# Kernel tuning notes

Measured on AMD Instinct MI355X. Metric: run time of the kernel, lower is better.

The kernel has to match this reference:

```python
import jax, jax.numpy as jnp
import numpy as np

N_NODES = 100000
N_GRAPHS = 64


def _gcn_norm(edge_index, num_nodes):
    # Add self-loops and compute symmetric normalization (PyG GCNConv gcn_norm).
    src = jnp.concatenate([edge_index[0], jnp.arange(num_nodes, dtype=edge_index.dtype)])
    dst = jnp.concatenate([edge_index[1], jnp.arange(num_nodes, dtype=edge_index.dtype)])
    deg = jax.ops.segment_sum(jnp.ones_like(dst, dtype=jnp.float32), dst, num_segments=num_nodes)
    dinv = jnp.where(deg > 0, jax.lax.rsqrt(deg), 0.0)
    norm = dinv[src] * dinv[dst]  # [E + N]
    return src, dst, norm


def _gcn_conv(x, src, dst, norm, W, b, num_nodes):
    h = x @ W                                   # [N, out]
    msg = h[src] * norm[:, None]                # gather + scale  [E+N, out]
    out = jax.ops.segment_sum(msg, dst, num_segments=num_nodes)  # scatter-add
    return out + b


def setup_inputs() -> dict:
    key = jax.random.key(0)
    ks = jax.random.split(key, 8)
    E = 1600000
    pos = jax.random.normal(ks[0], (N_NODES, 3), dtype=jnp.float32)
    edge_index = jax.random.randint(ks[1], (2, E), 0, N_NODES, dtype=jnp.int64)
    batch = jnp.sort(jax.random.randint(ks[2], (N_NODES,), 0, N_GRAPHS, dtype=jnp.int64))
    def glorot(k, shape):
        lim = np.sqrt(6.0 / (shape[0] + shape[1])).astype(np.float32)
        return jax.random.uniform(k, shape, dtype=jnp.float32, minval=-lim, maxval=lim)
    return {
        "pos": pos,
        "edge_index": edge_index,
        "batch": batch,
        "W1": glorot(ks[3], (3, 64)),  "b1": jnp.zeros((64,), jnp.float32),
        "W2": glorot(ks[4], (64, 64)), "b2": jnp.zeros((64,), jnp.float32),
        "W3": glorot(ks[5], (64, 24)), "b3": jnp.zeros((24,), jnp.float32),
    }


def reference(pos, edge_index, batch, W1, b1, W2, b2, W3, b3):
    src, dst, norm = _gcn_norm(edge_index, N_NODES)
    h = jax.nn.relu(_gcn_conv(pos, src, dst, norm, W1, b1, N_NODES))
    h = jax.nn.relu(_gcn_conv(h, src, dst, norm, W2, b2, N_NODES))
    y = _gcn_conv(h, src, dst, norm, W3, b3, N_NODES)  # [N, 24]
    # global_mean_pool over batch ids, then tanh
    sums = jax.ops.segment_sum(y, batch, num_segments=N_GRAPHS)          # [G, 24]
    counts = jax.ops.segment_sum(jnp.ones((N_NODES,), jnp.float32), batch, num_segments=N_GRAPHS)
    mean = sums / jnp.maximum(counts, 1.0)[:, None]
    return jnp.tanh(mean)
```

## Files before the change

### kernel.cpp

```cpp
#include <hip/hip_runtime.h>
#include <math.h>

#define NNODES 100000
#define NGRAPHS 64
#define NB 391
#define CAP 4608
#define NBLKA 1024
#define NBLKB 512


__device__ __forceinline__ unsigned int f2bf(float x) {
    union { float f; unsigned int u; } v;
    v.f = x;
    unsigned int r = v.u + 0x7FFFu + ((v.u >> 16) & 1u);
    return r >> 16;
}
__device__ __forceinline__ unsigned int pack2bf(float lo, float hi) {
    return f2bf(lo) | (f2bf(hi) << 16);
}
__device__ __forceinline__ float bflo(unsigned int u) {
    union { unsigned int u; float f; } v;
    v.u = u << 16;
    return v.f;
}
__device__ __forceinline__ float bfhi(unsigned int u) {
    union { unsigned int u; float f; } v;
    v.u = u & 0xFFFF0000u;
    return v.f;
}


__device__ __forceinline__ int ntld(const int* p) { return __builtin_nontemporal_load(p); }
__device__ __forceinline__ int2 ntld2(const int2* p) {
    long long v = __builtin_nontemporal_load((const long long*)p);
    int2 r;
    r.x = (int)(unsigned int)(v & 0xffffffffLL);
    r.y = (int)(v >> 32);
    return r;
}


__global__ void bucket_scatter(const int* __restrict__ src, const int* __restrict__ dst,
                               int* __restrict__ bCur, unsigned int* __restrict__ packed,
                               int E) {
    __shared__ int h[NB];
    __shared__ int cur[NB];
    for (int k = threadIdx.x; k < NB; k += 256) h[k] = 0;
    __syncthreads();
    int base = blockIdx.x * 2048 + threadIdx.x;
    int d[8], s[8], b[8];
#pragma unroll
    for (int k = 0; k < 8; ++k) {
        int e = base + k * 256;
        if (e < E) {
            d[k] = dst[e];
            s[k] = src[e];
            b[k] = d[k] >> 8;
            atomicAdd(&h[b[k]], 1);
        }
    }
    __syncthreads();
    for (int k = threadIdx.x; k < NB; k += 256) {
        int c = h[k];
        cur[k] = c ? atomicAdd(&bCur[k], c) : 0;
    }
    __syncthreads();
#pragma unroll
    for (int k = 0; k < 8; ++k) {
        int e = base + k * 256;
        if (e < E) {
            int pos = atomicAdd(&cur[b[k]], 1);
            if (pos < CAP)
                packed[(size_t)b[k] * CAP + pos] = ((unsigned int)(d[k] & 255) << 17) | (unsigned int)s[k];
        }
    }
}

__global__ void bucket_build(const unsigned int* __restrict__ packed, const int* __restrict__ bCur,
                             const int* __restrict__ batch, const float* __restrict__ pos,
                             int2* __restrict__ rowBE, int* __restrict__ col,
                             float* __restrict__ dinv, int2* __restrict__ dg,
                             float4* __restrict__ pos4, int N_) {
    __shared__ int cnt[256];
    __shared__ int bas[256];
    int tid = threadIdx.x;
    int b = blockIdx.x;
    int count = bCur[b];
    if (count > CAP) count = CAP;
    int beg = b * CAP;
    cnt[tid] = 0;
    __syncthreads();
    for (int k = beg + tid; k < beg + count; k += 256) atomicAdd(&cnt[packed[k] >> 17], 1);
    __syncthreads();
    int myCnt = cnt[tid];
    bas[tid] = myCnt;
    __syncthreads();
    for (int off = 1; off < 256; off <<= 1) {
        int v = (tid >= off) ? bas[tid - off] : 0;
        __syncthreads();
        bas[tid] += v;
        __syncthreads();
    }
    int excl = beg + ((tid > 0) ? bas[tid - 1] : 0);
    int node = (b << 8) + tid;
    if (node < N_) {
        rowBE[node] = make_int2(excl, excl + myCnt);
        float di = rsqrtf((float)myCnt + 1.0f);
        dinv[node] = di;
        dg[node] = make_int2(__float_as_int(di), batch[node]);
        pos4[node] = make_float4(pos[node * 3] * di, pos[node * 3 + 1] * di,
                                 pos[node * 3 + 2] * di, di);
    }
    __syncthreads();
    bas[tid] = excl;
    __syncthreads();
    for (int k = beg + tid; k < beg + count; k += 256) {
        unsigned int p = packed[k];
        int pos_ = atomicAdd(&bas[p >> 17], 1);
        col[pos_] = (int)(p & 0x1FFFFu);
    }
}


__global__ void mm12_gp(const float4* __restrict__ pos4, const int2* __restrict__ rowBE,
                        const int* __restrict__ col, const float* __restrict__ dinv,
                        const float* __restrict__ W1, const float* __restrict__ b1,
                        const float* __restrict__ W2, uint2* __restrict__ outb, int n) {
    __shared__ float4 part[256];
    __shared__ float4 ag[64];
    __shared__ float xs[64][65];
    __shared__ float4 ws[64 * 16];
    const int tid = threadIdx.x;
    const int rowBase = blockIdx.x * 64;
    const int r = tid >> 2, t4 = tid & 3;
    const int i = rowBase + r;

    float sx = 0, sy = 0, sz = 0, dival = 0;
    if (i < n) {
        int2 be = rowBE[i];
        float4 ps = pos4[i];
        dival = ps.w;
        if (t4 == 0) { sx = ps.x; sy = ps.y; sz = ps.z; }
        for (int j = be.x + t4; j < be.y; j += 4) {
            float4 v = pos4[ntld(&col[j])];
            sx += v.x; sy += v.y; sz += v.z;
        }
    }
    part[tid] = make_float4(sx, sy, sz, dival);
    const float4* W24 = (const float4*)W2;
    for (int idx = tid; idx < 64 * 16; idx += 256) ws[idx] = W24[idx];
    __syncthreads();
    if (tid < 64) {
        float4 p0 = part[tid * 4], p1 = part[tid * 4 + 1];
        float4 p2 = part[tid * 4 + 2], p3 = part[tid * 4 + 3];
        ag[tid] = make_float4((p0.x + p1.x) + (p2.x + p3.x),
                              (p0.y + p1.y) + (p2.y + p3.y),
                              (p0.z + p1.z) + (p2.z + p3.z), p0.w);
    }
    __syncthreads();
    for (int idx = tid; idx < 64 * 64; idx += 256) {
        int rr = idx >> 6;
        int k = idx & 63;
        float4 a = ag[rr];
        float v = b1[k] + a.w * (a.x * W1[k] + a.y * W1[64 + k] + a.z * W1[128 + k]);
        xs[rr][k] = fmaxf(v, 0.0f);
    }
    __syncthreads();

    const int f4 = tid & 15;
    const int r0 = (tid >> 4) * 4;
    float4 a0 = make_float4(0, 0, 0, 0), a1 = a0, a2 = a0, a3 = a0;
#pragma unroll 4
    for (int k = 0; k < 64; ++k) {
        float4 wv = ws[k * 16 + f4];
        float xa = xs[r0 + 0][k];
        float xb = xs[r0 + 1][k];
        float xc = xs[r0 + 2][k];
        float xd = xs[r0 + 3][k];
        a0.x += wv.x * xa; a0.y += wv.y * xa; a0.z += wv.z * xa; a0.w += wv.w * xa;
        a1.x += wv.x * xb; a1.y += wv.y * xb; a1.z += wv.z * xb; a1.w += wv.w * xb;
        a2.x += wv.x * xc; a2.y += wv.y * xc; a2.z += wv.z * xc; a2.w += wv.w * xc;
        a3.x += wv.x * xd; a3.y += wv.y * xd; a3.z += wv.z * xd; a3.w += wv.w * xd;
    }
    int i0 = rowBase + r0;
    float d0 = (i0 + 0 < n) ? dinv[i0 + 0] : 1.0f;
    float d1 = (i0 + 1 < n) ? dinv[i0 + 1] : 1.0f;
    float d2 = (i0 + 2 < n) ? dinv[i0 + 2] : 1.0f;
    float d3 = (i0 + 3 < n) ? dinv[i0 + 3] : 1.0f;
    if (i0 + 0 < n)
        outb[(size_t)(i0 + 0) * 16 + f4] = make_uint2(pack2bf(a0.x * d0, a0.y * d0), pack2bf(a0.z * d0, a0.w * d0));
    if (i0 + 1 < n)
        outb[(size_t)(i0 + 1) * 16 + f4] = make_uint2(pack2bf(a1.x * d1, a1.y * d1), pack2bf(a1.z * d1, a1.w * d1));
    if (i0 + 2 < n)
        outb[(size_t)(i0 + 2) * 16 + f4] = make_uint2(pack2bf(a2.x * d2, a2.y * d2), pack2bf(a2.z * d2, a2.w * d2));
    if (i0 + 3 < n)
        outb[(size_t)(i0 + 3) * 16 + f4] = make_uint2(pack2bf(a3.x * d3, a3.y * d3), pack2bf(a3.z * d3, a3.w * d3));
}


__global__ void gather2_b16(const int2* __restrict__ rowBE, const int* __restrict__ col,
                            const uint4* __restrict__ h, const float* __restrict__ dinv,
                            const float* __restrict__ bias, uint4* __restrict__ outb, int n) {
    int t = blockIdx.x * blockDim.x + threadIdx.x;
    if (t >= n * 8) return;
    int i = t >> 3;
    int c8 = t & 7;
    float di = dinv[i];
    int2 be = rowBE[i];
    float acc[8];
    {
        uint4 sv = h[t];
        acc[0] = bflo(sv.x); acc[1] = bfhi(sv.x);
        acc[2] = bflo(sv.y); acc[3] = bfhi(sv.y);
        acc[4] = bflo(sv.z); acc[5] = bfhi(sv.z);
        acc[6] = bflo(sv.w); acc[7] = bfhi(sv.w);
    }
    int j = be.x;
    for (; j + 8 <= be.y; j += 8) {
        int s[8];
        uint4 v[8];
#pragma unroll
        for (int k = 0; k < 8; ++k) s[k] = ntld(&col[j + k]);
#pragma unroll
        for (int k = 0; k < 8; ++k) v[k] = h[(size_t)s[k] * 8 + c8];
#pragma unroll
        for (int k = 0; k < 8; ++k) {
            acc[0] += bflo(v[k].x); acc[1] += bfhi(v[k].x);
            acc[2] += bflo(v[k].y); acc[3] += bfhi(v[k].y);
            acc[4] += bflo(v[k].z); acc[5] += bfhi(v[k].z);
            acc[6] += bflo(v[k].w); acc[7] += bfhi(v[k].w);
        }
    }
    for (; j < be.y; ++j) {
        uint4 v = h[(size_t)ntld(&col[j]) * 8 + c8];
        acc[0] += bflo(v.x); acc[1] += bfhi(v.x);
        acc[2] += bflo(v.y); acc[3] += bfhi(v.y);
        acc[4] += bflo(v.z); acc[5] += bfhi(v.z);
        acc[6] += bflo(v.w); acc[7] += bfhi(v.w);
    }
    const float* bv = bias + c8 * 8;
#pragma unroll
    for (int k = 0; k < 8; ++k) acc[k] = fmaxf(acc[k] * di + bv[k], 0.0f);
    outb[t] = make_uint4(pack2bf(acc[0], acc[1]), pack2bf(acc[2], acc[3]),
                         pack2bf(acc[4], acc[5]), pack2bf(acc[6], acc[7]));
}


__device__ __forceinline__ void st_y(uint2* __restrict__ yA, uint2* __restrict__ yB,
                                     int i, int f4, uint2 v) {
    if (f4 < 4) yA[(size_t)i * 4 + f4] = v;
    else        yB[(size_t)i * 2 + (f4 - 4)] = v;
}

__global__ void mm3_b16(const uint4* __restrict__ xb, const float* __restrict__ W,
                        const float* __restrict__ dinv, uint2* __restrict__ yA,
                        uint2* __restrict__ yB, int n) {
    __shared__ float xs[128][65];
    __shared__ float4 ws[64 * 6];
    const int tid = threadIdx.x;
    const int rowBase = blockIdx.x * 128;

    for (int idx = tid; idx < 128 * 8; idx += 192) {
        int r = idx >> 3;
        int c8 = idx & 7;
        int gr = rowBase + r;
        uint4 v = (gr < n) ? xb[(size_t)gr * 8 + c8] : make_uint4(0, 0, 0, 0);
        float* xp = &xs[r][c8 * 8];
        xp[0] = bflo(v.x); xp[1] = bfhi(v.x);
        xp[2] = bflo(v.y); xp[3] = bfhi(v.y);
        xp[4] = bflo(v.z); xp[5] = bfhi(v.z);
        xp[6] = bflo(v.w); xp[7] = bfhi(v.w);
    }
    const float4* W4 = (const float4*)W;
    for (int idx = tid; idx < 64 * 6; idx += 192) ws[idx] = W4[idx];
    __syncthreads();

    const int f4 = tid % 6;
    const int r0 = (tid / 6) * 4;
    float4 a0 = make_float4(0, 0, 0, 0), a1 = a0, a2 = a0, a3 = a0;
#pragma unroll 4
    for (int k = 0; k < 64; ++k) {
        float4 wv = ws[k * 6 + f4];
        float xa = xs[r0 + 0][k];
        float xb_ = xs[r0 + 1][k];
        float xc = xs[r0 + 2][k];
        float xd = xs[r0 + 3][k];
        a0.x += wv.x * xa; a0.y += wv.y * xa; a0.z += wv.z * xa; a0.w += wv.w * xa;
        a1.x += wv.x * xb_; a1.y += wv.y * xb_; a1.z += wv.z * xb_; a1.w += wv.w * xb_;
        a2.x += wv.x * xc; a2.y += wv.y * xc; a2.z += wv.z * xc; a2.w += wv.w * xc;
        a3.x += wv.x * xd; a3.y += wv.y * xd; a3.z += wv.z * xd; a3.w += wv.w * xd;
    }
    int i0 = rowBase + r0;
    float d0 = (i0 + 0 < n) ? dinv[i0 + 0] : 1.0f;
    float d1 = (i0 + 1 < n) ? dinv[i0 + 1] : 1.0f;
    float d2 = (i0 + 2 < n) ? dinv[i0 + 2] : 1.0f;
    float d3 = (i0 + 3 < n) ? dinv[i0 + 3] : 1.0f;
    if (i0 + 0 < n)
        st_y(yA, yB, i0 + 0, f4, make_uint2(pack2bf(a0.x * d0, a0.y * d0), pack2bf(a0.z * d0, a0.w * d0)));
    if (i0 + 1 < n)
        st_y(yA, yB, i0 + 1, f4, make_uint2(pack2bf(a1.x * d1, a1.y * d1), pack2bf(a1.z * d1, a1.w * d1)));
    if (i0 + 2 < n)
        st_y(yA, yB, i0 + 2, f4, make_uint2(pack2bf(a2.x * d2, a2.y * d2), pack2bf(a2.z * d2, a2.w * d2)));
    if (i0 + 3 < n)
        st_y(yA, yB, i0 + 3, f4, make_uint2(pack2bf(a3.x * d3, a3.y * d3), pack2bf(a3.z * d3, a3.w * d3)));
}


__global__ void gather3A(const int2* __restrict__ rowBE, const int* __restrict__ col,
                         const uint4* __restrict__ yA, const int2* __restrict__ dg,
                         float* __restrict__ partA) {
    __shared__ float lpool[NGRAPHS * 16];
    for (int k = threadIdx.x; k < NGRAPHS * 16; k += 256) lpool[k] = 0.0f;
    __syncthreads();

    const int T = NNODES * 4;
    const int stride = NBLKA * 256;
    for (int t = blockIdx.x * 256 + threadIdx.x; t < T; t += stride) {
        int i = t >> 2;
        int half = t & 1;
        int r = (t >> 1) & 1;
        int2 wi = ntld2(&dg[i]);
        float di = __int_as_float(wi.x);
        int g = wi.y;
        int2 be = ntld2(&rowBE[i]);
        int mid = be.x + ((be.y - be.x + 1) >> 1);
        int a = half ? mid : be.x;
        int b = half ? be.y : mid;
        float acc[8] = {0, 0, 0, 0, 0, 0, 0, 0};
        if (!half) {
            uint4 sv = yA[(size_t)i * 2 + r];
            acc[0] = bflo(sv.x); acc[1] = bfhi(sv.x);
            acc[2] = bflo(sv.y); acc[3] = bfhi(sv.y);
            acc[4] = bflo(sv.z); acc[5] = bfhi(sv.z);
            acc[6] = bflo(sv.w); acc[7] = bfhi(sv.w);
        }
        int j = a;
        for (; j + 8 <= b; j += 8) {
            int s[8];
            uint4 v[8];
#pragma unroll
            for (int k = 0; k < 8; ++k) s[k] = ntld(&col[j + k]);
#pragma unroll
            for (int k = 0; k < 8; ++k) v[k] = yA[(size_t)s[k] * 2 + r];
#pragma unroll
            for (int k = 0; k < 8; ++k) {
                acc[0] += bflo(v[k].x); acc[1] += bfhi(v[k].x);
                acc[2] += bflo(v[k].y); acc[3] += bfhi(v[k].y);
                acc[4] += bflo(v[k].z); acc[5] += bfhi(v[k].z);
                acc[6] += bflo(v[k].w); acc[7] += bfhi(v[k].w);
            }
        }
        for (; j < b; ++j) {
            uint4 v = yA[(size_t)ntld(&col[j]) * 2 + r];
            acc[0] += bflo(v.x); acc[1] += bfhi(v.x);
            acc[2] += bflo(v.y); acc[3] += bfhi(v.y);
            acc[4] += bflo(v.z); acc[5] += bfhi(v.z);
            acc[6] += bflo(v.w); acc[7] += bfhi(v.w);
        }
#pragma unroll
        for (int k = 0; k < 8; ++k) acc[k] += __shfl_xor(acc[k], 1);
        if (!half) {
            float* lp = &lpool[g * 16 + r * 8];
#pragma unroll
            for (int k = 0; k < 8; ++k) atomicAdd(&lp[k], acc[k] * di);
        }
    }
    __syncthreads();
    float* pp = partA + (size_t)blockIdx.x * (NGRAPHS * 16);
    for (int k = threadIdx.x; k < NGRAPHS * 16; k += 256) pp[k] = lpool[k];
}

__global__ void gather3B(const int2* __restrict__ rowBE, const int* __restrict__ col,
                         const uint4* __restrict__ yB, const int2* __restrict__ dg,
                         float* __restrict__ partB, float* __restrict__ cpart) {
    __shared__ float lpool[NGRAPHS * 8];
    __shared__ float lcnt[NGRAPHS];
    for (int k = threadIdx.x; k < NGRAPHS * 8; k += 256) lpool[k] = 0.0f;
    for (int k = threadIdx.x; k < NGRAPHS; k += 256) lcnt[k] = 0.0f;
    __syncthreads();

    const int T = NNODES * 2;
    const int stride = NBLKB * 256;
    for (int t = blockIdx.x * 256 + threadIdx.x; t < T; t += stride) {
        int i = t >> 1;
        int half = t & 1;
        int2 wi = ntld2(&dg[i]);
        float di = __int_as_float(wi.x);
        int g = wi.y;
        int2 be = ntld2(&rowBE[i]);
        int mid = be.x + ((be.y - be.x + 1) >> 1);
        int a = half ? mid : be.x;
        int b = half ? be.y : mid;
        float acc[8] = {0, 0, 0, 0, 0, 0, 0, 0};
        if (!half) {
            uint4 sv = yB[i];
            acc[0] = bflo(sv.x); acc[1] = bfhi(sv.x);
            acc[2] = bflo(sv.y); acc[3] = bfhi(sv.y);
            acc[4] = bflo(sv.z); acc[5] = bfhi(sv.z);
            acc[6] = bflo(sv.w); acc[7] = bfhi(sv.w);
        }
        int j = a;
        for (; j + 8 <= b; j += 8) {
            int s[8];
            uint4 v[8];
#pragma unroll
            for (int k = 0; k < 8; ++k) s[k] = ntld(&col[j + k]);
#pragma unroll
            for (int k = 0; k < 8; ++k) v[k] = yB[s[k]];
#pragma unroll
            for (int k = 0; k < 8; ++k) {
                acc[0] += bflo(v[k].x); acc[1] += bfhi(v[k].x);
                acc[2] += bflo(v[k].y); acc[3] += bfhi(v[k].y);
                acc[4] += bflo(v[k].z); acc[5] += bfhi(v[k].z);
                acc[6] += bflo(v[k].w); acc[7] += bfhi(v[k].w);
            }
        }
        for (; j < b; ++j) {
            uint4 v = yB[ntld(&col[j])];
            acc[0] += bflo(v.x); acc[1] += bfhi(v.x);
            acc[2] += bflo(v.y); acc[3] += bfhi(v.y);
            acc[4] += bflo(v.z); acc[5] += bfhi(v.z);
            acc[6] += bflo(v.w); acc[7] += bfhi(v.w);
        }
#pragma unroll
        for (int k = 0; k < 8; ++k) acc[k] += __shfl_xor(acc[k], 1);
        if (!half) {
            float* lp = &lpool[g * 8];
#pragma unroll
            for (int k = 0; k < 8; ++k) atomicAdd(&lp[k], acc[k] * di);
            atomicAdd(&lcnt[g], 1.0f);
        }
    }
    __syncthreads();
    float* pp = partB + (size_t)blockIdx.x * (NGRAPHS * 8);
    for (int k = threadIdx.x; k < NGRAPHS * 8; k += 256) pp[k] = lpool[k];
    float* cp = cpart + (size_t)blockIdx.x * NGRAPHS;
    for (int k = threadIdx.x; k < NGRAPHS; k += 256) cp[k] = lcnt[k];
}

__global__ void pool_finish(const float* __restrict__ partA, const float* __restrict__ partB,
                            const float* __restrict__ cpart, const float* __restrict__ b3,
                            float* __restrict__ out) {
    int w = blockIdx.x * 4 + (threadIdx.x >> 6);
    int lane = threadIdx.x & 63;
    if (w >= NGRAPHS * 24) return;
    int g = w / 24;
    int c = w - g * 24;
    float s = 0.0f, cn = 0.0f;
    if (c < 16) {
        for (int b = lane; b < NBLKA; b += 64) s += partA[(size_t)b * (NGRAPHS * 16) + g * 16 + c];
    } else {
        for (int b = lane; b < NBLKB; b += 64) s += partB[(size_t)b * (NGRAPHS * 8) + g * 8 + (c - 16)];
    }
    for (int b = lane; b < NBLKB; b += 64) cn += cpart[(size_t)b * NGRAPHS + g];
#pragma unroll
    for (int off = 32; off > 0; off >>= 1) {
        s += __shfl_down(s, off);
        cn += __shfl_down(cn, off);
    }
    if (lane == 0) out[w] = tanhf(s / fmaxf(cn, 1.0f) + b3[c]);
}


static inline int gridFor(long long total, int block) {
    return (int)((total + block - 1) / block);
}

extern "C" void kernel_launch(void* const* d_in, const int* in_sizes, int n_in,
                              void* d_out, int out_size, void* d_ws, size_t ws_size,
                              hipStream_t stream) {
    const float* pos   = (const float*)d_in[0];
    const int*   ei    = (const int*)d_in[1];
    const int*   batch = (const int*)d_in[2];
    const float* W1    = (const float*)d_in[3];
    const float* b1    = (const float*)d_in[4];
    const float* W2    = (const float*)d_in[5];
    const float* b2    = (const float*)d_in[6];
    const float* W3    = (const float*)d_in[7];
    const float* b3    = (const float*)d_in[8];
    float*       out   = (float*)d_out;

    const int N = NNODES;
    const int E = in_sizes[1] / 2;
    const int* src = ei;
    const int* dst = ei + E;

    char* p = (char*)d_ws;
    uint4*  z2b    = (uint4*)p;         p += (size_t)N * 8 * sizeof(uint4);
    uint4*  h2b    = (uint4*)p;         p += (size_t)N * 8 * sizeof(uint4);
    uint4*  yA     = (uint4*)p;         p += (size_t)N * 2 * sizeof(uint4);
    uint4*  yB     = (uint4*)p;         p += (size_t)N * 1 * sizeof(uint4);
    float4* pos4   = (float4*)p;        p += (size_t)N * sizeof(float4);
    int2*   rowBE  = (int2*)p;          p += (size_t)N * sizeof(int2);
    int2*   dg     = (int2*)p;          p += (size_t)N * sizeof(int2);
    float*  dinv   = (float*)p;         p += (size_t)N * sizeof(float);
    int*    bCur   = (int*)p;           p += NB * sizeof(int);
    unsigned int* packed = (unsigned int*)p;  p += (size_t)NB * CAP * sizeof(unsigned int);
    int*    col    = (int*)p;           p += (size_t)NB * CAP * sizeof(int);
    float*  partA  = (float*)z2b;
    float*  partB  = partA + (size_t)NBLKA * NGRAPHS * 16;
    float*  cpartB = partB + (size_t)NBLKB * NGRAPHS * 8;

    const int B = 256;
    const int edgeBlocks = gridFor(E, 2048);

    hipMemsetAsync(bCur, 0, NB * sizeof(int), stream);
    bucket_scatter<<<edgeBlocks, 256, 0, stream>>>(src, dst, bCur, packed, E);
    bucket_build<<<NB, 256, 0, stream>>>(packed, bCur, batch, pos, rowBE, col, dinv, dg, pos4, N);

    mm12_gp<<<gridFor(N, 64), 256, 0, stream>>>(pos4, rowBE, col, dinv, W1, b1, W2, (uint2*)z2b, N);

    gather2_b16<<<gridFor((long long)N * 8, B), B, 0, stream>>>(rowBE, col, z2b, dinv, b2, h2b, N);

    mm3_b16<<<gridFor(N, 128), 192, 0, stream>>>(h2b, W3, dinv, (uint2*)yA, (uint2*)yB, N);
    gather3A<<<NBLKA, 256, 0, stream>>>(rowBE, col, yA, dg, partA);
    gather3B<<<NBLKB, 256, 0, stream>>>(rowBE, col, yB, dg, partB, cpartB);
    pool_finish<<<gridFor((long long)NGRAPHS * 24 * 64, B), B, 0, stream>>>(partA, partB, cpartB, b3, out);
}
```

Measured before the change: 265.3 us.

## Fuse layer-2 gather with layer-3 matmul via shared-memory tile

Merges the layer-2 neighbor aggregation and the layer-3 64x24 projection into one kernel. Each 256-thread block aggregates 32 nodes, writes the ReLU outputs to shared memory, then 192 threads compute the W3 projection and store the bf16 yA/yB outputs. This drops the h2b intermediate's global write and reread and one kernel launch. In exchange it adds a block barrier after the irregular gather and a small per-block W3 load, and it removes the bounds check, which relies on N*8 being a multiple of 256.

After: 256.9 us, median of 3. 1.03x faster.

```diff
diff --git a/kernel.cpp b/kernel.cpp
--- a/kernel.cpp
+++ b/kernel.cpp
@@ -198,15 +198,28 @@
 }
 
 
-__global__ void gather2_b16(const int2* __restrict__ rowBE, const int* __restrict__ col,
+__device__ __forceinline__ void st_y(uint2* __restrict__ yA, uint2* __restrict__ yB,
+                                     int i, int f4, uint2 v) {
+    if (f4 < 4) yA[(size_t)i * 4 + f4] = v;
+    else        yB[(size_t)i * 2 + (f4 - 4)] = v;
+}
+
+__global__ void gather2_mm3(const int2* __restrict__ rowBE, const int* __restrict__ col,
                             const uint4* __restrict__ h, const float* __restrict__ dinv,
-                            const float* __restrict__ bias, uint4* __restrict__ outb, int n) {
-    int t = blockIdx.x * blockDim.x + threadIdx.x;
-    if (t >= n * 8) return;
-    int i = t >> 3;
-    int c8 = t & 7;
-    float di = dinv[i];
-    int2 be = rowBE[i];
+                            const float* __restrict__ bias, const float* __restrict__ W3,
+                            uint2* __restrict__ yA, uint2* __restrict__ yB) {
+    __shared__ float hs[32][65];
+    __shared__ float dd[32];
+    __shared__ float w3s[64 * 24];
+    const int tid = threadIdx.x;
+    for (int idx = tid; idx < 64 * 24 / 4; idx += 256)
+        ((float4*)w3s)[idx] = ((const float4*)W3)[idx];
+
+    const int t = blockIdx.x * 256 + tid;
+    const int i = t >> 3;
+    const int c8 = t & 7;
+    const float di = dinv[i];
+    const int2 be = rowBE[i];
     float acc[8];
     {
         uint4 sv = h[t];
@@ -238,71 +251,35 @@
         acc[4] += bflo(v.z); acc[5] += bfhi(v.z);
         acc[6] += bflo(v.w); acc[7] += bfhi(v.w);
     }
-    const float* bv = bias + c8 * 8;
-#pragma unroll
-    for (int k = 0; k < 8; ++k) acc[k] = fmaxf(acc[k] * di + bv[k], 0.0f);
-    outb[t] = make_uint4(pack2bf(acc[0], acc[1]), pack2bf(acc[2], acc[3]),
-                         pack2bf(acc[4], acc[5]), pack2bf(acc[6], acc[7]));
-}
-
-
-__device__ __forceinline__ void st_y(uint2* __restrict__ yA, uint2* __restrict__ yB,
-                                     int i, int f4, uint2 v) {
-    if (f4 < 4) yA[(size_t)i * 4 + f4] = v;
-    else        yB[(size_t)i * 2 + (f4 - 4)] = v;
-}
-
-__global__ void mm3_b16(const uint4* __restrict__ xb, const float* __restrict__ W,
-                        const float* __restrict__ dinv, uint2* __restrict__ yA,
-                        uint2* __restrict__ yB, int n) {
-    __shared__ float xs[128][65];
-    __shared__ float4 ws[64 * 6];
-    const int tid = threadIdx.x;
-    const int rowBase = blockIdx.x * 128;
-
-    for (int idx = tid; idx < 128 * 8; idx += 192) {
-        int r = idx >> 3;
-        int c8 = idx & 7;
-        int gr = rowBase + r;
-        uint4 v = (gr < n) ? xb[(size_t)gr * 8 + c8] : make_uint4(0, 0, 0, 0);
-        float* xp = &xs[r][c8 * 8];
-        xp[0] = bflo(v.x); xp[1] = bfhi(v.x);
-        xp[2] = bflo(v.y); xp[3] = bfhi(v.y);
-        xp[4] = bflo(v.z); xp[5] = bfhi(v.z);
-        xp[6] = bflo(v.w); xp[7] = bfhi(v.w);
-    }
-    const float4* W4 = (const float4*)W;
-    for (int idx = tid; idx < 64 * 6; idx += 192) ws[idx] = W4[idx];
-    __syncthreads();
-
-    const int f4 = tid % 6;
-    const int r0 = (tid / 6) * 4;
-    float4 a0 = make_float4(0, 0, 0, 0), a1 = a0, a2 = a0, a3 = a0;
+    const int il = tid >> 3;
+    {
+        const float* bv = bias + c8 * 8;
+        float* hp = &hs[il][c8 * 8];
+#pragma unroll
+        for (int k = 0; k < 8; ++k) hp[k] = fmaxf(acc[k] * di + bv[k], 0.0f);
+        if (c8 == 0) dd[il] = di;
+    }
+    __syncthreads();
+
+    if (tid < 192) {
+        const int node = tid / 6;
+        const int f4 = tid - node * 6;
+        const int gi = blockIdx.x * 32 + node;
+        const float dloc = dd[node];
+        const float* hrow = hs[node];
+        const float* wp = &w3s[f4 * 4];
+        float c0 = 0, c1 = 0, c2 = 0, c3 = 0;
 #pragma unroll 4
-    for (int k = 0; k < 64; ++k) {
-        float4 wv = ws[k * 6 + f4];
-        float xa = xs[r0 + 0][k];
-        float xb_ = xs[r0 + 1][k];
-        float xc = xs[r0 + 2][k];
-        float xd = xs[r0 + 3][k];
-        a0.x += wv.x * xa; a0.y += wv.y * xa; a0.z += wv.z * xa; a0.w += wv.w * xa;
-        a1.x += wv.x * xb_; a1.y += wv.y * xb_; a1.z += wv.z * xb_; a1.w += wv.w * xb_;
-        a2.x += wv.x * xc; a2.y += wv.y * xc; a2.z += wv.z * xc; a2.w += wv.w * xc;
-        a3.x += wv.x * xd; a3.y += wv.y * xd; a3.z += wv.z * xd; a3.w += wv.w * xd;
-    }
-    int i0 = rowBase + r0;
-    float d0 = (i0 + 0 < n) ? dinv[i0 + 0] : 1.0f;
-    float d1 = (i0 + 1 < n) ? dinv[i0 + 1] : 1.0f;
-    float d2 = (i0 + 2 < n) ? dinv[i0 + 2] : 1.0f;
-    float d3 = (i0 + 3 < n) ? dinv[i0 + 3] : 1.0f;
-    if (i0 + 0 < n)
-        st_y(yA, yB, i0 + 0, f4, make_uint2(pack2bf(a0.x * d0, a0.y * d0), pack2bf(a0.z * d0, a0.w * d0)));
-    if (i0 + 1 < n)
-        st_y(yA, yB, i0 + 1, f4, make_uint2(pack2bf(a1.x * d1, a1.y * d1), pack2bf(a1.z * d1, a1.w * d1)));
-    if (i0 + 2 < n)
-        st_y(yA, yB, i0 + 2, f4, make_uint2(pack2bf(a2.x * d2, a2.y * d2), pack2bf(a2.z * d2, a2.w * d2)));
-    if (i0 + 3 < n)
-        st_y(yA, yB, i0 + 3, f4, make_uint2(pack2bf(a3.x * d3, a3.y * d3), pack2bf(a3.z * d3, a3.w * d3)));
+        for (int k = 0; k < 64; ++k) {
+            float hv = hrow[k];
+            c0 += hv * wp[k * 24 + 0];
+            c1 += hv * wp[k * 24 + 1];
+            c2 += hv * wp[k * 24 + 2];
+            c3 += hv * wp[k * 24 + 3];
+        }
+        st_y(yA, yB, gi, f4, make_uint2(pack2bf(c0 * dloc, c1 * dloc),
+                                        pack2bf(c2 * dloc, c3 * dloc)));
+    }
 }
 
 
@@ -487,7 +464,6 @@
 
     char* p = (char*)d_ws;
     uint4*  z2b    = (uint4*)p;         p += (size_t)N * 8 * sizeof(uint4);
-    uint4*  h2b    = (uint4*)p;         p += (size_t)N * 8 * sizeof(uint4);
     uint4*  yA     = (uint4*)p;         p += (size_t)N * 2 * sizeof(uint4);
     uint4*  yB     = (uint4*)p;         p += (size_t)N * 1 * sizeof(uint4);
     float4* pos4   = (float4*)p;        p += (size_t)N * sizeof(float4);
@@ -510,9 +486,9 @@
 
     mm12_gp<<<gridFor(N, 64), 256, 0, stream>>>(pos4, rowBE, col, dinv, W1, b1, W2, (uint2*)z2b, N);
 
-    gather2_b16<<<gridFor((long long)N * 8, B), B, 0, stream>>>(rowBE, col, z2b, dinv, b2, h2b, N);
-
-    mm3_b16<<<gridFor(N, 128), 192, 0, stream>>>(h2b, W3, dinv, (uint2*)yA, (uint2*)yB, N);
+    gather2_mm3<<<gridFor((long long)N * 8, B), B, 0, stream>>>(rowBE, col, z2b, dinv, b2, W3,
+                                                                (uint2*)yA, (uint2*)yB);
+
     gather3A<<<NBLKA, 256, 0, stream>>>(rowBE, col, yA, dg, partA);
     gather3B<<<NBLKB, 256, 0, stream>>>(rowBE, col, yB, dg, partB, cpartB);
     pool_finish<<<gridFor((long long)NGRAPHS * 24 * 64, B), B, 0, stream>>>(partA, partB, cpartB, b3, out);
```

## Slice layer-2 features into four 16-channel planes for cache-local gathers

Applied to the files above, without the earlier changes.

The layer-2 intermediate is stored as four separate 16-channel bf16 planes, each node-major, instead of one interleaved 64-channel row. The new gather kernel processes one plane per grid slice, with four threads per node splitting the edge list and reducing through shuffles. Each plane is 3.2 MB, so the random neighbour gathers can hit in cache instead of streaming the full 12.8 MB array. The cost is reading the edge list four times and an extra shuffle reduction. The producer mm12 and consumer mm3 kernels are updated to the sliced layout.

Result: slower. 287.6 us (+8.4%).

```diff
diff --git a/kernel.cpp b/kernel.cpp
--- a/kernel.cpp
+++ b/kernel.cpp
@@ -7,6 +7,7 @@
 #define CAP 4608
 #define NBLKA 1024
 #define NBLKB 512
+#define NT2 1563
 
 
 __device__ __forceinline__ unsigned int f2bf(float x) {
@@ -28,6 +29,12 @@
     v.u = u & 0xFFFF0000u;
     return v.f;
 }
+
+#define ACC8(A, ofs, V) \
+    A[(ofs) + 0] += bflo((V).x); A[(ofs) + 1] += bfhi((V).x); \
+    A[(ofs) + 2] += bflo((V).y); A[(ofs) + 3] += bfhi((V).y); \
+    A[(ofs) + 4] += bflo((V).z); A[(ofs) + 5] += bfhi((V).z); \
+    A[(ofs) + 6] += bflo((V).w); A[(ofs) + 7] += bfhi((V).w);
 
 
 __device__ __forceinline__ int ntld(const int* p) { return __builtin_nontemporal_load(p); }
@@ -125,7 +132,7 @@
 __global__ void mm12_gp(const float4* __restrict__ pos4, const int2* __restrict__ rowBE,
                         const int* __restrict__ col, const float* __restrict__ dinv,
                         const float* __restrict__ W1, const float* __restrict__ b1,
-                        const float* __restrict__ W2, uint2* __restrict__ outb, int n) {
+                        const float* __restrict__ W2, uint2* __restrict__ outz, int n) {
     __shared__ float4 part[256];
     __shared__ float4 ag[64];
     __shared__ float xs[64][65];
@@ -187,62 +194,78 @@
     float d1 = (i0 + 1 < n) ? dinv[i0 + 1] : 1.0f;
     float d2 = (i0 + 2 < n) ? dinv[i0 + 2] : 1.0f;
     float d3 = (i0 + 3 < n) ? dinv[i0 + 3] : 1.0f;
+    const size_t gsel = (size_t)(f4 >> 2) * NNODES;
+    const int sub = f4 & 3;
     if (i0 + 0 < n)
-        outb[(size_t)(i0 + 0) * 16 + f4] = make_uint2(pack2bf(a0.x * d0, a0.y * d0), pack2bf(a0.z * d0, a0.w * d0));
+        outz[(gsel + (i0 + 0)) * 4 + sub] = make_uint2(pack2bf(a0.x * d0, a0.y * d0), pack2bf(a0.z * d0, a0.w * d0));
     if (i0 + 1 < n)
-        outb[(size_t)(i0 + 1) * 16 + f4] = make_uint2(pack2bf(a1.x * d1, a1.y * d1), pack2bf(a1.z * d1, a1.w * d1));
+        outz[(gsel + (i0 + 1)) * 4 + sub] = make_uint2(pack2bf(a1.x * d1, a1.y * d1), pack2bf(a1.z * d1, a1.w * d1));
     if (i0 + 2 < n)
-        outb[(size_t)(i0 + 2) * 16 + f4] = make_uint2(pack2bf(a2.x * d2, a2.y * d2), pack2bf(a2.z * d2, a2.w * d2));
+        outz[(gsel + (i0 + 2)) * 4 + sub] = make_uint2(pack2bf(a2.x * d2, a2.y * d2), pack2bf(a2.z * d2, a2.w * d2));
     if (i0 + 3 < n)
-        outb[(size_t)(i0 + 3) * 16 + f4] = make_uint2(pack2bf(a3.x * d3, a3.y * d3), pack2bf(a3.z * d3, a3.w * d3));
-}
-
-
-__global__ void gather2_b16(const int2* __restrict__ rowBE, const int* __restrict__ col,
-                            const uint4* __restrict__ h, const float* __restrict__ dinv,
-                            const float* __restrict__ bias, uint4* __restrict__ outb, int n) {
-    int t = blockIdx.x * blockDim.x + threadIdx.x;
-    if (t >= n * 8) return;
-    int i = t >> 3;
-    int c8 = t & 7;
-    float di = dinv[i];
-    int2 be = rowBE[i];
-    float acc[8];
-    {
-        uint4 sv = h[t];
-        acc[0] = bflo(sv.x); acc[1] = bfhi(sv.x);
-        acc[2] = bflo(sv.y); acc[3] = bfhi(sv.y);
-        acc[4] = bflo(sv.z); acc[5] = bfhi(sv.z);
-        acc[6] = bflo(sv.w); acc[7] = bfhi(sv.w);
-    }
-    int j = be.x;
-    for (; j + 8 <= be.y; j += 8) {
-        int s[8];
-        uint4 v[8];
-#pragma unroll
-        for (int k = 0; k < 8; ++k) s[k] = ntld(&col[j + k]);
-#pragma unroll
-        for (int k = 0; k < 8; ++k) v[k] = h[(size_t)s[k] * 8 + c8];
-#pragma unroll
-        for (int k = 0; k < 8; ++k) {
-            acc[0] += bflo(v[k].x); acc[1] += bfhi(v[k].x);
-            acc[2] += bflo(v[k].y); acc[3] += bfhi(v[k].y);
-            acc[4] += bflo(v[k].z); acc[5] += bfhi(v[k].z);
-            acc[6] += bflo(v[k].w); acc[7] += bfhi(v[k].w);
-        }
-    }
-    for (; j < be.y; ++j) {
-        uint4 v = h[(size_t)ntld(&col[j]) * 8 + c8];
-        acc[0] += bflo(v.x); acc[1] += bfhi(v.x);
-        acc[2] += bflo(v.y); acc[3] += bfhi(v.y);
-        acc[4] += bflo(v.z); acc[5] += bfhi(v.z);
-        acc[6] += bflo(v.w); acc[7] += bfhi(v.w);
-    }
-    const float* bv = bias + c8 * 8;
-#pragma unroll
-    for (int k = 0; k < 8; ++k) acc[k] = fmaxf(acc[k] * di + bv[k], 0.0f);
-    outb[t] = make_uint4(pack2bf(acc[0], acc[1]), pack2bf(acc[2], acc[3]),
-                         pack2bf(acc[4], acc[5]), pack2bf(acc[6], acc[7]));
+        outz[(gsel + (i0 + 3)) * 4 + sub] = make_uint2(pack2bf(a3.x * d3, a3.y * d3), pack2bf(a3.z * d3, a3.w * d3));
+}
+
+
+__global__ void gather2_sliced(const int2* __restrict__ rowBE, const int* __restrict__ col,
+                               const uint4* __restrict__ z2s, const float* __restrict__ dinv,
+                               const float* __restrict__ b2, uint4* __restrict__ h2s) {
+    const int tid = threadIdx.x;
+    const int g = blockIdx.x / NT2;
+    const int tile = blockIdx.x - g * NT2;
+    const int il = tid >> 2, t4 = tid & 3;
+    const int i = tile * 64 + il;
+    const size_t base = (size_t)g * NNODES;
+
+    float acc[16];
+#pragma unroll
+    for (int k = 0; k < 16; ++k) acc[k] = 0.0f;
+
+    if (i < NNODES) {
+        if (t4 == 0) {
+            uint4 sa = z2s[(base + i) * 2 + 0];
+            uint4 sb = z2s[(base + i) * 2 + 1];
+            ACC8(acc, 0, sa)
+            ACC8(acc, 8, sb)
+        }
+        int2 be = rowBE[i];
+        int j = be.x + t4;
+        for (; j + 4 < be.y; j += 8) {
+            int s0 = ntld(&col[j]);
+            int s1 = ntld(&col[j + 4]);
+            uint4 a0 = z2s[(base + s0) * 2 + 0];
+            uint4 b0 = z2s[(base + s0) * 2 + 1];
+            uint4 a1 = z2s[(base + s1) * 2 + 0];
+            uint4 b1 = z2s[(base + s1) * 2 + 1];
+            ACC8(acc, 0, a0)
+            ACC8(acc, 8, b0)
+            ACC8(acc, 0, a1)
+            ACC8(acc, 8, b1)
+        }
+        for (; j < be.y; j += 4) {
+            int s = ntld(&col[j]);
+            uint4 a = z2s[(base + s) * 2 + 0];
+            uint4 b = z2s[(base + s) * 2 + 1];
+            ACC8(acc, 0, a)
+            ACC8(acc, 8, b)
+        }
+    }
+#pragma unroll
+    for (int k = 0; k < 16; ++k) acc[k] += __shfl_xor(acc[k], 1);
+#pragma unroll
+    for (int k = 0; k < 16; ++k) acc[k] += __shfl_xor(acc[k], 2);
+
+    if (t4 == 0 && i < NNODES) {
+        float di = dinv[i];
+        const float* bv = b2 + g * 16;
+        float h[16];
+#pragma unroll
+        for (int k = 0; k < 16; ++k) h[k] = fmaxf(acc[k] * di + bv[k], 0.0f);
+        h2s[(base + i) * 2 + 0] = make_uint4(pack2bf(h[0], h[1]), pack2bf(h[2], h[3]),
+                                             pack2bf(h[4], h[5]), pack2bf(h[6], h[7]));
+        h2s[(base + i) * 2 + 1] = make_uint4(pack2bf(h[8], h[9]), pack2bf(h[10], h[11]),
+                                             pack2bf(h[12], h[13]), pack2bf(h[14], h[15]));
+    }
 }
 
 
@@ -264,7 +287,8 @@
         int r = idx >> 3;
         int c8 = idx & 7;
         int gr = rowBase + r;
-        uint4 v = (gr < n) ? xb[(size_t)gr * 8 + c8] : make_uint4(0, 0, 0, 0);
+        uint4 v = (gr < n) ? xb[((size_t)(c8 >> 1) * NNODES + gr) * 2 + (c8 & 1)]
+                           : make_uint4(0, 0, 0, 0);
         float* xp = &xs[r][c8 * 8];
         xp[0] = bflo(v.x); xp[1] = bfhi(v.x);
         xp[2] = bflo(v.y); xp[3] = bfhi(v.y);
@@ -486,8 +510,8 @@
     const int* dst = ei + E;
 
     char* p = (char*)d_ws;
-    uint4*  z2b    = (uint4*)p;         p += (size_t)N * 8 * sizeof(uint4);
-    uint4*  h2b    = (uint4*)p;         p += (size_t)N * 8 * sizeof(uint4);
+    uint4*  z2s    = (uint4*)p;         p += (size_t)N * 8 * sizeof(uint4);
+    uint4*  h2s    = (uint4*)p;         p += (size_t)N * 8 * sizeof(uint4);
     uint4*  yA     = (uint4*)p;         p += (size_t)N * 2 * sizeof(uint4);
     uint4*  yB     = (uint4*)p;         p += (size_t)N * 1 * sizeof(uint4);
     float4* pos4   = (float4*)p;        p += (size_t)N * sizeof(float4);
@@ -497,7 +521,7 @@
     int*    bCur   = (int*)p;           p += NB * sizeof(int);
     unsigned int* packed = (unsigned int*)p;  p += (size_t)NB * CAP * sizeof(unsigned int);
     int*    col    = (int*)p;           p += (size_t)NB * CAP * sizeof(int);
-    float*  partA  = (float*)z2b;
+    float*  partA  = (float*)z2s;
     float*  partB  = partA + (size_t)NBLKA * NGRAPHS * 16;
     float*  cpartB = partB + (size_t)NBLKB * NGRAPHS * 8;
 
@@ -508,11 +532,12 @@
     bucket_scatter<<<edgeBlocks, 256, 0, stream>>>(src, dst, bCur, packed, E);
     bucket_build<<<NB, 256, 0, stream>>>(packed, bCur, batch, pos, rowBE, col, dinv, dg, pos4, N);
 
-    mm12_gp<<<gridFor(N, 64), 256, 0, stream>>>(pos4, rowBE, col, dinv, W1, b1, W2, (uint2*)z2b, N);
-
-    gather2_b16<<<gridFor((long long)N * 8, B), B, 0, stream>>>(rowBE, col, z2b, dinv, b2, h2b, N);
-
-    mm3_b16<<<gridFor(N, 128), 192, 0, stream>>>(h2b, W3, dinv, (uint2*)yA, (uint2*)yB, N);
+    mm12_gp<<<gridFor(N, 64), 256, 0, stream>>>(pos4, rowBE, col, dinv, W1, b1, W2, (uint2*)z2s, N);
+
+    gather2_sliced<<<4 * NT2, 256, 0, stream>>>(rowBE, col, z2s, dinv, b2, h2s);
+
+    mm3_b16<<<gridFor(N, 128), 192, 0, stream>>>(h2s, W3, dinv, (uint2*)yA, (uint2*)yB, N);
+
     gather3A<<<NBLKA, 256, 0, stream>>>(rowBE, col, yA, dg, partA);
     gather3B<<<NBLKB, 256, 0, stream>>>(rowBE, col, yB, dg, partB, cpartB);
     pool_finish<<<gridFor((long long)NGRAPHS * 24 * 64, B), B, 0, stream>>>(partA, partB, cpartB, b3, out);
```
